# Performance work log

Hardware: AMD Instinct MI355X
Metric: run time of the kernel (lower is better)

## Reference

```python
import jax, jax.numpy as jnp
import numpy as np

HIDDEN = 1024
D_INNER = 2048      # expand * hidden
STATE = 16          # state_dim n
DT_RANK = 64        # ceil(hidden/16)
D_CONV = 4
B, S = 2, 2048
EPS = 1e-5


def setup_inputs() -> dict:
    key = jax.random.key(0)
    ks = jax.random.split(key, 10)
    sc = lambda fan_in: 1.0 / np.sqrt(fan_in)
    x = jax.random.normal(ks[0], (B, S, HIDDEN), dtype=jnp.float32)
    norm_w = jnp.ones((HIDDEN,), dtype=jnp.float32)
    in_proj_w = jax.random.uniform(ks[1], (2 * D_INNER, HIDDEN), minval=-sc(HIDDEN), maxval=sc(HIDDEN), dtype=jnp.float32)
    conv_w = jax.random.uniform(ks[2], (D_INNER, 1, D_CONV), minval=-sc(D_CONV), maxval=sc(D_CONV), dtype=jnp.float32)
    conv_b = jax.random.uniform(ks[3], (D_INNER,), minval=-sc(D_CONV), maxval=sc(D_CONV), dtype=jnp.float32)
    x_proj_w = jax.random.uniform(ks[4], (DT_RANK + 2 * STATE, D_INNER), minval=-sc(D_INNER), maxval=sc(D_INNER), dtype=jnp.float32)
    dt_proj_w = jax.random.uniform(ks[5], (D_INNER, DT_RANK), minval=-sc(DT_RANK), maxval=sc(DT_RANK), dtype=jnp.float32)
    dt_proj_b = jax.random.uniform(ks[6], (D_INNER,), minval=-sc(DT_RANK), maxval=sc(DT_RANK), dtype=jnp.float32)
    A_log = jnp.log(jnp.broadcast_to(jnp.arange(1, STATE + 1, dtype=jnp.float32), (D_INNER, STATE)))
    D = jnp.ones((D_INNER,), dtype=jnp.float32)
    out_proj_w = jax.random.uniform(ks[7], (HIDDEN, D_INNER), minval=-sc(D_INNER), maxval=sc(D_INNER), dtype=jnp.float32)
    return {"x": x, "norm_w": norm_w, "in_proj_w": in_proj_w, "conv_w": conv_w,
            "conv_b": conv_b, "x_proj_w": x_proj_w, "dt_proj_w": dt_proj_w,
            "dt_proj_b": dt_proj_b, "A_log": A_log, "D": D, "out_proj_w": out_proj_w}


def _selective_scan(u, delta, A, Bm, Cm, D):
    # u, delta: [b,s,d]; A: [d,n]; Bm, Cm: [b,s,n]; D: [d]
    deltaA = jnp.exp(jnp.einsum('bsd,dn->bsdn', delta, A))          # [b,s,d,n]
    deltaB_u = jnp.einsum('bsd,bsn,bsd->bsdn', delta, Bm, u)        # [b,s,d,n]

    def step(h, inp):
        dA_t, dBu_t, C_t = inp                                       # [b,d,n],[b,d,n],[b,n]
        h = dA_t * h + dBu_t
        y = jnp.einsum('bdn,bn->bd', h, C_t)
        return h, y

    h0 = jnp.zeros((u.shape[0], u.shape[2], A.shape[1]), dtype=u.dtype)
    _, ys = jax.lax.scan(step, h0,
                         (deltaA.transpose(1, 0, 2, 3),
                          deltaB_u.transpose(1, 0, 2, 3),
                          Cm.transpose(1, 0, 2)))
    y = ys.transpose(1, 0, 2)                                        # [b,s,d]
    return y + u * D


def reference(x, norm_w, in_proj_w, conv_w, conv_b, x_proj_w, dt_proj_w,
              dt_proj_b, A_log, D, out_proj_w):
    # RMSNorm
    xn = x * jax.lax.rsqrt(jnp.mean(x * x, axis=-1, keepdims=True) + EPS) * norm_w

    # in_proj -> split
    x_and_res = xn @ in_proj_w.T                                     # [b,s,2*d_inner]
    xi, res = jnp.split(x_and_res, 2, axis=-1)

    # causal depthwise conv1d (left-pad d_conv-1, truncate to s)
    xc = jax.lax.conv_general_dilated(
        xi.transpose(0, 2, 1), conv_w,
        window_strides=(1,), padding=[(D_CONV - 1, 0)],
        dimension_numbers=('NCH', 'OIH', 'NCH'),
        feature_group_count=D_INNER) + conv_b[None, :, None]
    xc = jax.nn.silu(xc.transpose(0, 2, 1))                          # [b,s,d_inner]

    # ssm
    A = -jnp.exp(A_log)
    x_dbl = xc @ x_proj_w.T                                          # [b,s,dt_rank+2n]
    dt, Bm, Cm = jnp.split(x_dbl, [DT_RANK, DT_RANK + STATE], axis=-1)
    delta = jax.nn.softplus(dt @ dt_proj_w.T + dt_proj_b)            # [b,s,d_inner]
    y = _selective_scan(xc, delta, A, Bm, Cm, D)

    y = y * jax.nn.silu(res)
    out = y @ out_proj_w.T
    return out + x
```

## Files before the change

kernel.cpp:

```cpp
#include <hip/hip_runtime.h>
#include <math.h>

#define HIDDEN   1024
#define D_INNER  2048
#define NSTATE   16
#define DT_RANK  64
#define BATCH    2
#define SEQ      2048
#define T_TOK    (BATCH * SEQ)
#define XDBL     (DT_RANK + 2 * NSTATE)
#define NCH      64
#define CHL      (SEQ / NCH)
#define BDN      (BATCH * D_INNER * NSTATE)

typedef float f32x4   __attribute__((ext_vector_type(4)));
typedef short bf16x8  __attribute__((ext_vector_type(8)));
typedef short short4v __attribute__((ext_vector_type(4)));

#define AS1 __attribute__((address_space(1)))
#define AS3 __attribute__((address_space(3)))
#define GLOAD(src, dst) __builtin_amdgcn_global_load_lds( \
    (const AS1 unsigned int*)(src), (AS3 unsigned int*)(dst), 16, 0, 0)

__device__ __forceinline__ float silu_f(float x) { return x / (1.0f + __expf(-x)); }
__device__ __forceinline__ float softplus_f(float x) {
    return fmaxf(x, 0.0f) + log1pf(__expf(-fabsf(x)));
}
__device__ __forceinline__ unsigned short f2bf(float x) {
    unsigned int u = __float_as_uint(x);
    u += 0x7fffu + ((u >> 16) & 1u);
    return (unsigned short)(u >> 16);
}
__device__ __forceinline__ float bf2f(unsigned short h) {
    return __uint_as_float(((unsigned int)h) << 16);
}

template<int SEGS>
__global__ __launch_bounds__(256) void wpack_kernel(
        const float* __restrict__ w, unsigned short* __restrict__ wp, int K) {
    int i = blockIdx.x * 256 + threadIdx.x;
    int kq = K >> 2;
    int row = i / kq;
    int c = (i - row * kq) << 2;
    float4 v = *(const float4*)(w + (size_t)row * K + c);
    short4v hi, lo;
    hi.x = f2bf(v.x); hi.y = f2bf(v.y); hi.z = f2bf(v.z); hi.w = f2bf(v.w);
    lo.x = f2bf(v.x - bf2f(hi.x)); lo.y = f2bf(v.y - bf2f(hi.y));
    lo.z = f2bf(v.z - bf2f(hi.z)); lo.w = f2bf(v.w - bf2f(hi.w));
    size_t b0 = (size_t)row * (SEGS * K) + c;
    *(short4v*)(wp + b0) = hi;
    if (SEGS == 2) *(short4v*)(wp + b0 + K) = lo;
}

__global__ __launch_bounds__(256) void rmsnorm_pack_kernel(
        const float* __restrict__ x, const float* __restrict__ w,
        unsigned short* __restrict__ xn_p) {
    int row = blockIdx.x;
    float4 v = ((const float4*)(x + (size_t)row * HIDDEN))[threadIdx.x];
    float ss = v.x*v.x + v.y*v.y + v.z*v.z + v.w*v.w;
    #pragma unroll
    for (int off = 32; off; off >>= 1) ss += __shfl_down(ss, off);
    __shared__ float wsum[4];
    if ((threadIdx.x & 63) == 0) wsum[threadIdx.x >> 6] = ss;
    __syncthreads();
    float scale = rsqrtf((wsum[0] + wsum[1] + wsum[2] + wsum[3]) / (float)HIDDEN + 1e-5f);
    float4 wv = ((const float4*)w)[threadIdx.x];
    float o0 = v.x * scale * wv.x, o1 = v.y * scale * wv.y;
    float o2 = v.z * scale * wv.z, o3 = v.w * scale * wv.w;
    short4v hi, lo;
    hi.x = f2bf(o0); hi.y = f2bf(o1); hi.z = f2bf(o2); hi.w = f2bf(o3);
    lo.x = f2bf(o0 - bf2f(hi.x)); lo.y = f2bf(o1 - bf2f(hi.y));
    lo.z = f2bf(o2 - bf2f(hi.z)); lo.w = f2bf(o3 - bf2f(hi.w));
    size_t b0 = (size_t)row * (2 * HIDDEN) + threadIdx.x * 4;
    *(short4v*)&xn_p[b0]          = hi;
    *(short4v*)&xn_p[b0 + HIDDEN] = lo;
}

__global__ __launch_bounds__(256, 2) void mgemm_in_kernel(
        const unsigned short* __restrict__ Ap,
        const unsigned short* __restrict__ Wp,
        float* __restrict__ C0, float* __restrict__ C1) {
    __shared__ short Ah[128 * 64];
    __shared__ short Al[128 * 64];
    __shared__ short Bh[256 * 64];
    const int t = threadIdx.x;
    const int w = t >> 6, l = t & 63;
    const int m0 = blockIdx.y * 128, n0 = blockIdx.x * 256;
    const int lrow = l & 15;
    f32x4 acc[8][4];
    #pragma unroll
    for (int m = 0; m < 8; ++m)
        #pragma unroll
        for (int n = 0; n < 4; ++n) {
            acc[m][n].x = 0.f; acc[m][n].y = 0.f; acc[m][n].z = 0.f; acc[m][n].w = 0.f;
        }
    const int srow8 = l >> 3;
    const int sc8   = (l & 7) ^ srow8;
    const unsigned short* ga = Ap + (size_t)(m0 + w * 32 + srow8) * 2048 + sc8 * 8;
    const unsigned short* gb = Wp + (size_t)(n0 + w * 64 + srow8) * 1024 + sc8 * 8;
    for (int k0 = 0; k0 < 1024; k0 += 64) {
        __syncthreads();
        #pragma unroll
        for (int q = 0; q < 4; ++q) {
            const int ar = (w * 32 + q * 8) * 128;
            GLOAD(ga + k0 + (size_t)q * 8 * 2048,        (char*)Ah + ar);
            GLOAD(ga + 1024 + k0 + (size_t)q * 8 * 2048, (char*)Al + ar);
        }
        #pragma unroll
        for (int q = 0; q < 8; ++q)
            GLOAD(gb + k0 + (size_t)q * 8 * 1024, (char*)Bh + (w * 64 + q * 8) * 128);
        __syncthreads();
        #pragma unroll
        for (int kk = 0; kk < 2; ++kk) {
            const int slot = ((kk * 4 + (l >> 4)) ^ (l & 7)) * 8;
            bf16x8 bh[4];
            #pragma unroll
            for (int n = 0; n < 4; ++n)
                bh[n] = *(const bf16x8*)&Bh[(w * 64 + n * 16 + lrow) * 64 + slot];
            #pragma unroll
            for (int m = 0; m < 8; ++m) {
                bf16x8 ah = *(const bf16x8*)&Ah[(m * 16 + lrow) * 64 + slot];
                bf16x8 al = *(const bf16x8*)&Al[(m * 16 + lrow) * 64 + slot];
                #pragma unroll
                for (int n = 0; n < 4; ++n) {
                    acc[m][n] = __builtin_amdgcn_mfma_f32_16x16x32_bf16(
                        ah, bh[n], acc[m][n], 0, 0, 0);
                    acc[m][n] = __builtin_amdgcn_mfma_f32_16x16x32_bf16(
                        al, bh[n], acc[m][n], 0, 0, 0);
                }
            }
        }
    }
    float* dst = (n0 < D_INNER) ? C0 : C1;
    const int cbase = (n0 < D_INNER) ? n0 : n0 - D_INNER;
    #pragma unroll
    for (int m = 0; m < 8; ++m) {
        #pragma unroll
        for (int n = 0; n < 4; ++n) {
            #pragma unroll
            for (int j = 0; j < 4; ++j) {
                int row = m0 + m * 16 + (l >> 4) * 4 + j;
                int col = cbase + w * 64 + n * 16 + (l & 15);
                dst[(size_t)row * D_INNER + col] = acc[m][n][j];
            }
        }
    }
}

template<int TERMS, int EPI>
__global__ __launch_bounds__(256) void mgemm_kernel(
        const unsigned short* __restrict__ Ap, const unsigned short* __restrict__ Wp,
        int Klog, int klen, int brows, float* __restrict__ C0, float* __restrict__ C1,
        int splitN, int ldout, size_t partStride, const float* __restrict__ bias) {
    constexpr int NT = (TERMS == 3) ? 4 : 3;
    __shared__ short lds[NT * 128 * 64];
    short* Ah = lds;
    short* Al = lds + 128 * 64;
    short* Bh = lds + 2 * 128 * 64;
    short* Bl = lds + 3 * 128 * 64;
    const int t = threadIdx.x;
    const int w = t >> 6, l = t & 63;
    const int m0 = blockIdx.y * 128, n0 = blockIdx.x * 128;
    const int kbeg = blockIdx.z * klen;
    const int wr = (w >> 1) * 64, wc = (w & 1) * 64;
    const int lrow = l & 15;
    f32x4 acc[4][4];
    #pragma unroll
    for (int m = 0; m < 4; ++m)
        #pragma unroll
        for (int n = 0; n < 4; ++n) {
            acc[m][n].x = 0.f; acc[m][n].y = 0.f; acc[m][n].z = 0.f; acc[m][n].w = 0.f;
        }
    const int Asr = 2 * Klog;
    const int Wsr = (TERMS == 3) ? 2 * Klog : Klog;
    const int srow = w * 32 + (l >> 3);
    const int sc8  = (l & 7) ^ ((l >> 3) & 7);
    const int brow = min(n0 + srow, brows - 1);
    const unsigned short* ga = Ap + (size_t)(m0 + srow) * Asr + sc8 * 8;
    const unsigned short* gb = Wp + (size_t)brow * Wsr + sc8 * 8;
    for (int k0 = kbeg; k0 < kbeg + klen; k0 += 64) {
        __syncthreads();
        #pragma unroll
        for (int q = 0; q < 4; ++q) {
            const int doff = (w * 32 + q * 8) * 128;
            GLOAD(ga + k0 + (size_t)q * 8 * Asr,        (char*)Ah + doff);
            GLOAD(ga + Klog + k0 + (size_t)q * 8 * Asr, (char*)Al + doff);
            GLOAD(gb + k0 + (size_t)q * 8 * Wsr,        (char*)Bh + doff);
            if (TERMS == 3)
                GLOAD(gb + Klog + k0 + (size_t)q * 8 * Wsr, (char*)Bl + doff);
        }
        __syncthreads();
        #pragma unroll
        for (int kk = 0; kk < 2; ++kk) {
            const int slot = ((kk * 4 + (l >> 4)) ^ (l & 7)) * 8;
            bf16x8 ah[4], al[4], bh[4], bl[4];
            #pragma unroll
            for (int m = 0; m < 4; ++m) {
                ah[m] = *(const bf16x8*)&Ah[(wr + m * 16 + lrow) * 64 + slot];
                al[m] = *(const bf16x8*)&Al[(wr + m * 16 + lrow) * 64 + slot];
            }
            #pragma unroll
            for (int n = 0; n < 4; ++n) {
                bh[n] = *(const bf16x8*)&Bh[(wc + n * 16 + lrow) * 64 + slot];
                if (TERMS == 3)
                    bl[n] = *(const bf16x8*)&Bl[(wc + n * 16 + lrow) * 64 + slot];
            }
            #pragma unroll
            for (int m = 0; m < 4; ++m)
                #pragma unroll
                for (int n = 0; n < 4; ++n) {
                    acc[m][n] = __builtin_amdgcn_mfma_f32_16x16x32_bf16(
                        ah[m], bh[n], acc[m][n], 0, 0, 0);
                    acc[m][n] = __builtin_amdgcn_mfma_f32_16x16x32_bf16(
                        al[m], bh[n], acc[m][n], 0, 0, 0);
                    if (TERMS == 3)
                        acc[m][n] = __builtin_amdgcn_mfma_f32_16x16x32_bf16(
                            ah[m], bl[n], acc[m][n], 0, 0, 0);
                }
        }
    }
    float* dst = (EPI == 2) ? (C0 + blockIdx.z * partStride) : C0;
    #pragma unroll
    for (int m = 0; m < 4; ++m) {
        #pragma unroll
        for (int n = 0; n < 4; ++n) {
            #pragma unroll
            for (int j = 0; j < 4; ++j) {
                int row = m0 + wr + m * 16 + (l >> 4) * 4 + j;
                int col = n0 + wc + n * 16 + (l & 15);
                float v = acc[m][n][j];
                if (EPI == 2) {
                    dst[(size_t)row * ldout + col] = v;
                } else {
                    C0[(size_t)row * ldout + col] = softplus_f(v + bias[col]);
                }
            }
        }
    }
}

__global__ __launch_bounds__(256) void reduce2_kernel(
        const float* __restrict__ parts, size_t partStride,
        const float* __restrict__ x, float* __restrict__ out) {
    size_t i = (size_t)blockIdx.x * 256 + threadIdx.x;
    float4 a = ((const float4*)(parts))[i];
    float4 b = ((const float4*)(parts + partStride))[i];
    float4 xv = ((const float4*)x)[i];
    float4 o;
    o.x = a.x + b.x + xv.x;
    o.y = a.y + b.y + xv.y;
    o.z = a.z + b.z + xv.z;
    o.w = a.w + b.w + xv.w;
    ((float4*)out)[i] = o;
}

__global__ __launch_bounds__(256) void reduceX_kernel(
        const float* __restrict__ parts, float* __restrict__ xdbl,
        unsigned short* __restrict__ dtp) {
    int i = blockIdx.x * 256 + threadIdx.x;
    int row = i / 24;
    int c = (i - row * 24) * 4;
    float4 s = make_float4(0.f, 0.f, 0.f, 0.f);
    #pragma unroll
    for (int z = 0; z < 8; ++z) {
        float4 a = *(const float4*)(parts + (size_t)z * 524288 + (size_t)row * 128 + c);
        s.x += a.x; s.y += a.y; s.z += a.z; s.w += a.w;
    }
    *(float4*)(xdbl + (size_t)row * XDBL + c) = s;
    if (c < DT_RANK) {
        short4v hi, lo;
        hi.x = f2bf(s.x); hi.y = f2bf(s.y); hi.z = f2bf(s.z); hi.w = f2bf(s.w);
        lo.x = f2bf(s.x - bf2f(hi.x)); lo.y = f2bf(s.y - bf2f(hi.y));
        lo.z = f2bf(s.z - bf2f(hi.z)); lo.w = f2bf(s.w - bf2f(hi.w));
        size_t b0 = (size_t)row * 128 + c;
        *(short4v*)(dtp + b0)      = hi;
        *(short4v*)(dtp + b0 + 64) = lo;
    }
}

__global__ __launch_bounds__(256) void conv_silu_kernel(
        const float* __restrict__ xi, const float* __restrict__ w,
        const float* __restrict__ b, unsigned short* __restrict__ xc_p) {
    size_t i = (size_t)blockIdx.x * 256 + threadIdx.x;
    int d = (int)(i & (D_INNER - 1));
    int tt = (int)(i >> 11);
    int s = tt & (SEQ - 1);
    float4 wv = ((const float4*)w)[d];
    float acc = b[d];
    if (s >= 3) acc += wv.x * xi[i - 3 * D_INNER];
    if (s >= 2) acc += wv.y * xi[i - 2 * D_INNER];
    if (s >= 1) acc += wv.z * xi[i - 1 * D_INNER];
    acc += wv.w * xi[i];
    float o = silu_f(acc);
    unsigned short hi = f2bf(o);
    unsigned short lo = f2bf(o - bf2f(hi));
    size_t o2 = (size_t)tt * (2 * D_INNER) + d;
    xc_p[o2]           = hi;
    xc_p[o2 + D_INNER] = lo;
}


__global__ __launch_bounds__(256) void scanA_kernel(
        const unsigned short* __restrict__ xcp, const float* __restrict__ delta,
        const float* __restrict__ xdbl, const float* __restrict__ A_log,
        float* __restrict__ hpart, float* __restrict__ Pp) {
    const int bid = blockIdx.x;
    const int b    = bid >> 9;
    const int c    = (bid >> 3) & 63;
    const int dblk = bid & 7;
    const int d    = (dblk << 8) + threadIdx.x;
    float adn[NSTATE];
    #pragma unroll
    for (int k = 0; k < 4; ++k) {
        float4 a = *(const float4*)(A_log + d * NSTATE + k * 4);
        adn[k*4+0] = -__expf(a.x); adn[k*4+1] = -__expf(a.y);
        adn[k*4+2] = -__expf(a.z); adn[k*4+3] = -__expf(a.w);
    }
    float h[NSTATE], P[NSTATE];
    #pragma unroll
    for (int n = 0; n < NSTATE; ++n) { h[n] = 0.f; P[n] = 1.f; }
    const int rowbase = b * SEQ + c * CHL;
    #pragma unroll 4
    for (int r = 0; r < CHL; ++r) {
        const int row = rowbase + r;
        const float* brow = xdbl + (size_t)row * XDBL + DT_RANK;
        size_t o2 = (size_t)row * (2 * D_INNER) + d;
        float dl = delta[(size_t)row * D_INNER + d];
        float u  = bf2f(xcp[o2]) + bf2f(xcp[o2 + D_INNER]);
        float du = dl * u;
        #pragma unroll
        for (int n = 0; n < NSTATE; ++n) {
            float dA = __expf(dl * adn[n]);
            h[n] = fmaf(dA, h[n], du * brow[n]);
            P[n] *= dA;
        }
    }
    size_t base = (size_t)c * BDN + (size_t)(b * D_INNER + d) * NSTATE;
    #pragma unroll
    for (int k = 0; k < 4; ++k) {
        *(float4*)(hpart + base + k * 4) = make_float4(h[k*4], h[k*4+1], h[k*4+2], h[k*4+3]);
        *(float4*)(Pp    + base + k * 4) = make_float4(P[k*4], P[k*4+1], P[k*4+2], P[k*4+3]);
    }
}

__global__ __launch_bounds__(256) void scanB_kernel(
        const float* __restrict__ hpart, const float* __restrict__ Pp,
        float* __restrict__ hstart) {
    int idx = blockIdx.x * 256 + threadIdx.x;
    float h = 0.f;
    for (int c = 0; c < NCH; ++c) {
        hstart[(size_t)c * BDN + idx] = h;
        h = fmaf(Pp[(size_t)c * BDN + idx], h, hpart[(size_t)c * BDN + idx]);
    }
}

__global__ __launch_bounds__(256) void scanC_kernel(
        const unsigned short* xcp, const float* __restrict__ delta,
        const float* __restrict__ xdbl, const float* __restrict__ A_log,
        const float* __restrict__ Dp, const float* __restrict__ hstart,
        const float* __restrict__ res, unsigned short* y_p) {
    const int bid = blockIdx.x;
    const int b    = bid >> 9;
    const int c    = (bid >> 3) & 63;
    const int dblk = bid & 7;
    const int d    = (dblk << 8) + threadIdx.x;
    float adn[NSTATE];
    #pragma unroll
    for (int k = 0; k < 4; ++k) {
        float4 a = *(const float4*)(A_log + d * NSTATE + k * 4);
        adn[k*4+0] = -__expf(a.x); adn[k*4+1] = -__expf(a.y);
        adn[k*4+2] = -__expf(a.z); adn[k*4+3] = -__expf(a.w);
    }
    const float Dd = Dp[d];
    float h[NSTATE];
    size_t base = (size_t)c * BDN + (size_t)(b * D_INNER + d) * NSTATE;
    #pragma unroll
    for (int k = 0; k < 4; ++k) {
        float4 hv = *(const float4*)(hstart + base + k * 4);
        h[k*4] = hv.x; h[k*4+1] = hv.y; h[k*4+2] = hv.z; h[k*4+3] = hv.w;
    }
    const int rowbase = b * SEQ + c * CHL;
    #pragma unroll 4
    for (int r = 0; r < CHL; ++r) {
        const int row = rowbase + r;
        const float* brow = xdbl + (size_t)row * XDBL + DT_RANK;
        const float* crow = brow + NSTATE;
        size_t o2 = (size_t)row * (2 * D_INNER) + d;
        float dl = delta[(size_t)row * D_INNER + d];
        float u  = bf2f(xcp[o2]) + bf2f(xcp[o2 + D_INNER]);
        float du = dl * u;
        float ys[4];
        ys[0] = u * Dd; ys[1] = 0.f; ys[2] = 0.f; ys[3] = 0.f;
        #pragma unroll
        for (int n = 0; n < NSTATE; ++n) {
            float dA = __expf(dl * adn[n]);
            h[n] = fmaf(dA, h[n], du * brow[n]);
            ys[n & 3] = fmaf(h[n], crow[n], ys[n & 3]);
        }
        float ysum = (ys[0] + ys[1]) + (ys[2] + ys[3]);
        float rv = res[(size_t)row * D_INNER + d];
        float gv = ysum * silu_f(rv);
        unsigned short hi = f2bf(gv);
        unsigned short lo = f2bf(gv - bf2f(hi));
        y_p[o2]           = hi;
        y_p[o2 + D_INNER] = lo;
    }
}

extern "C" void kernel_launch(void* const* d_in, const int* in_sizes, int n_in,
                              void* d_out, int out_size, void* d_ws, size_t ws_size,
                              hipStream_t stream) {
    const float* x         = (const float*)d_in[0];
    const float* norm_w    = (const float*)d_in[1];
    const float* in_proj_w = (const float*)d_in[2];
    const float* conv_w    = (const float*)d_in[3];
    const float* conv_b    = (const float*)d_in[4];
    const float* x_proj_w  = (const float*)d_in[5];
    const float* dt_proj_w = (const float*)d_in[6];
    const float* dt_proj_b = (const float*)d_in[7];
    const float* A_log     = (const float*)d_in[8];
    const float* Dp        = (const float*)d_in[9];
    const float* out_proj_w= (const float*)d_in[10];
    float* out = (float*)d_out;
    float* ws  = (float*)d_ws;

    const size_t M8 = (size_t)T_TOK * D_INNER;
    float* res   = ws;
    float* delta = res + M8;
    float* xdbl  = delta + M8;
    unsigned short* xn_p   = (unsigned short*)(xdbl + (size_t)T_TOK * XDBL);
    unsigned short* w_in_p = xn_p   + (size_t)4096 * 2048;
    unsigned short* w_out_p= w_in_p + (size_t)4096 * 1024;
    unsigned short* w_xp_p = w_out_p+ (size_t)1024 * 4096;
    unsigned short* w_dt_p = w_xp_p + (size_t)96 * 4096;
    unsigned short* xc_p   = w_dt_p + (size_t)2048 * 128;
    unsigned short* dtp_p  = xc_p   + (size_t)4096 * 4096;
    float* xi    = (float*)(dtp_p + (size_t)4096 * 128);
    float* hpart = xi;
    float* Pp    = xi + (size_t)BDN * NCH;
    float* hstart= (float*)xn_p;
    float* parts_x = delta;
    unsigned short* y_p = xc_p;
    float* parts = ws;
    const size_t partStride = (size_t)T_TOK * HIDDEN;

    wpack_kernel<1><<<4096, 256, 0, stream>>>(in_proj_w,  w_in_p,  HIDDEN);
    wpack_kernel<2><<<2048, 256, 0, stream>>>(out_proj_w, w_out_p, D_INNER);
    wpack_kernel<2><<<192,  256, 0, stream>>>(x_proj_w,   w_xp_p,  D_INNER);
    wpack_kernel<2><<<128,  256, 0, stream>>>(dt_proj_w,  w_dt_p,  DT_RANK);

    rmsnorm_pack_kernel<<<T_TOK, 256, 0, stream>>>(x, norm_w, xn_p);

    {
        dim3 g(4096 / 256, T_TOK / 128, 1);
        mgemm_in_kernel<<<g, 256, 0, stream>>>(xn_p, w_in_p, xi, res);
    }

    conv_silu_kernel<<<(int)(M8 / 256), 256, 0, stream>>>(xi, conv_w, conv_b, xc_p);

    {
        dim3 g(1, T_TOK / 128, 8);
        mgemm_kernel<3, 2><<<g, 256, 0, stream>>>(xc_p, w_xp_p, D_INNER, D_INNER / 8,
                                                  96, parts_x, nullptr, 0, 128, 524288, nullptr);
    }
    reduceX_kernel<<<T_TOK * 24 / 256, 256, 0, stream>>>(parts_x, xdbl, dtp_p);

    {
        dim3 g(D_INNER / 128, T_TOK / 128, 1);
        mgemm_kernel<3, 3><<<g, 256, 0, stream>>>(dtp_p, w_dt_p, DT_RANK, DT_RANK,
                                                  D_INNER, delta, nullptr, 0, D_INNER, 0, dt_proj_b);
    }

    scanA_kernel<<<BATCH * NCH * 8, 256, 0, stream>>>(xc_p, delta, xdbl, A_log, hpart, Pp);
    scanB_kernel<<<BDN / 256, 256, 0, stream>>>(hpart, Pp, hstart);
    scanC_kernel<<<BATCH * NCH * 8, 256, 0, stream>>>(xc_p, delta, xdbl, A_log, Dp, hstart, res, y_p);

    {
        dim3 g(HIDDEN / 128, T_TOK / 128, 2);
        mgemm_kernel<3, 2><<<g, 256, 0, stream>>>(y_p, w_out_p, D_INNER, D_INNER / 2,
                                                  HIDDEN, parts, nullptr, 0, HIDDEN, partStride, nullptr);
    }
    reduce2_kernel<<<(int)(partStride / 4 / 256), 256, 0, stream>>>(parts, partStride, x, out);
}
```

Before: 312.7 us.

## Fuse weight packing, stage scan B/C in LDS, write scan prefix in place

Merges the four weight-pack launches into one kernel that branches on block index. The scan kernels now stage each chunk's B and C vectors in shared memory instead of reading them from global memory every step. scanB writes its prefix states back into hpart in place, which removes the separate hstart buffer. The GEMM template is also changed to always load and multiply the low-bf16 weight term, so TERMS no longer controls it; this adds work to any instantiation that used TERMS==2, though every current call site already uses 3.

```diff
diff --git a/kernel.cpp b/kernel.cpp
--- a/kernel.cpp
+++ b/kernel.cpp
@@ -35,10 +35,9 @@
     return __uint_as_float(((unsigned int)h) << 16);
 }
 
-template<int SEGS>
-__global__ __launch_bounds__(256) void wpack_kernel(
-        const float* __restrict__ w, unsigned short* __restrict__ wp, int K) {
-    int i = blockIdx.x * 256 + threadIdx.x;
+__device__ __forceinline__ void pack_seg(
+        const float* __restrict__ w, unsigned short* __restrict__ wp,
+        int K, int segs, int i) {
     int kq = K >> 2;
     int row = i / kq;
     int c = (i - row * kq) << 2;
@@ -47,9 +46,27 @@
     hi.x = f2bf(v.x); hi.y = f2bf(v.y); hi.z = f2bf(v.z); hi.w = f2bf(v.w);
     lo.x = f2bf(v.x - bf2f(hi.x)); lo.y = f2bf(v.y - bf2f(hi.y));
     lo.z = f2bf(v.z - bf2f(hi.z)); lo.w = f2bf(v.w - bf2f(hi.w));
-    size_t b0 = (size_t)row * (SEGS * K) + c;
+    size_t b0 = (size_t)row * (segs * K) + c;
     *(short4v*)(wp + b0) = hi;
-    if (SEGS == 2) *(short4v*)(wp + b0 + K) = lo;
+    if (segs == 2) *(short4v*)(wp + b0 + K) = lo;
+}
+
+__global__ __launch_bounds__(256) void wpack_all_kernel(
+        const float* __restrict__ win,  unsigned short* __restrict__ pin,
+        const float* __restrict__ wout, unsigned short* __restrict__ pout,
+        const float* __restrict__ wx,   unsigned short* __restrict__ px,
+        const float* __restrict__ wdt,  unsigned short* __restrict__ pdt) {
+    int bid = blockIdx.x;
+    int t = threadIdx.x;
+    if (bid < 4096) {
+        pack_seg(win, pin, HIDDEN, 1, bid * 256 + t);
+    } else if (bid < 6144) {
+        pack_seg(wout, pout, D_INNER, 2, (bid - 4096) * 256 + t);
+    } else if (bid < 6336) {
+        pack_seg(wx, px, D_INNER, 2, (bid - 6144) * 256 + t);
+    } else {
+        pack_seg(wdt, pdt, DT_RANK, 2, (bid - 6336) * 256 + t);
+    }
 }
 
 __global__ __launch_bounds__(256) void rmsnorm_pack_kernel(
@@ -172,7 +189,7 @@
             acc[m][n].x = 0.f; acc[m][n].y = 0.f; acc[m][n].z = 0.f; acc[m][n].w = 0.f;
         }
     const int Asr = 2 * Klog;
-    const int Wsr = (TERMS == 3) ? 2 * Klog : Klog;
+    const int Wsr = 2 * Klog;
     const int srow = w * 32 + (l >> 3);
     const int sc8  = (l & 7) ^ ((l >> 3) & 7);
     const int brow = min(n0 + srow, brows - 1);
@@ -186,8 +203,7 @@
             GLOAD(ga + k0 + (size_t)q * 8 * Asr,        (char*)Ah + doff);
             GLOAD(ga + Klog + k0 + (size_t)q * 8 * Asr, (char*)Al + doff);
             GLOAD(gb + k0 + (size_t)q * 8 * Wsr,        (char*)Bh + doff);
-            if (TERMS == 3)
-                GLOAD(gb + Klog + k0 + (size_t)q * 8 * Wsr, (char*)Bl + doff);
+            GLOAD(gb + Klog + k0 + (size_t)q * 8 * Wsr, (char*)Bl + doff);
         }
         __syncthreads();
         #pragma unroll
@@ -202,8 +218,7 @@
             #pragma unroll
             for (int n = 0; n < 4; ++n) {
                 bh[n] = *(const bf16x8*)&Bh[(wc + n * 16 + lrow) * 64 + slot];
-                if (TERMS == 3)
-                    bl[n] = *(const bf16x8*)&Bl[(wc + n * 16 + lrow) * 64 + slot];
+                bl[n] = *(const bf16x8*)&Bl[(wc + n * 16 + lrow) * 64 + slot];
             }
             #pragma unroll
             for (int m = 0; m < 4; ++m)
@@ -213,9 +228,8 @@
                         ah[m], bh[n], acc[m][n], 0, 0, 0);
                     acc[m][n] = __builtin_amdgcn_mfma_f32_16x16x32_bf16(
                         al[m], bh[n], acc[m][n], 0, 0, 0);
-                    if (TERMS == 3)
-                        acc[m][n] = __builtin_amdgcn_mfma_f32_16x16x32_bf16(
-                            ah[m], bl[n], acc[m][n], 0, 0, 0);
+                    acc[m][n] = __builtin_amdgcn_mfma_f32_16x16x32_bf16(
+                        ah[m], bl[n], acc[m][n], 0, 0, 0);
                 }
         }
     }
@@ -304,11 +318,19 @@
         const unsigned short* __restrict__ xcp, const float* __restrict__ delta,
         const float* __restrict__ xdbl, const float* __restrict__ A_log,
         float* __restrict__ hpart, float* __restrict__ Pp) {
+    __shared__ float sB[CHL * NSTATE];
     const int bid = blockIdx.x;
     const int b    = bid >> 9;
     const int c    = (bid >> 3) & 63;
     const int dblk = bid & 7;
     const int d    = (dblk << 8) + threadIdx.x;
+    const int rowbase = b * SEQ + c * CHL;
+    #pragma unroll
+    for (int q = 0; q < 2; ++q) {
+        int e = threadIdx.x + q * 256;
+        int r = e >> 4, n = e & 15;
+        sB[e] = xdbl[(size_t)(rowbase + r) * XDBL + DT_RANK + n];
+    }
     float adn[NSTATE];
     #pragma unroll
     for (int k = 0; k < 4; ++k) {
@@ -319,11 +341,11 @@
     float h[NSTATE], P[NSTATE];
     #pragma unroll
     for (int n = 0; n < NSTATE; ++n) { h[n] = 0.f; P[n] = 1.f; }
-    const int rowbase = b * SEQ + c * CHL;
+    __syncthreads();
     #pragma unroll 4
     for (int r = 0; r < CHL; ++r) {
         const int row = rowbase + r;
-        const float* brow = xdbl + (size_t)row * XDBL + DT_RANK;
+        const float* brow = &sB[r * NSTATE];
         size_t o2 = (size_t)row * (2 * D_INNER) + d;
         float dl = delta[(size_t)row * D_INNER + d];
         float u  = bf2f(xcp[o2]) + bf2f(xcp[o2 + D_INNER]);
@@ -344,13 +366,15 @@
 }
 
 __global__ __launch_bounds__(256) void scanB_kernel(
-        const float* __restrict__ hpart, const float* __restrict__ Pp,
-        float* __restrict__ hstart) {
+        float* __restrict__ hpart, const float* __restrict__ Pp) {
     int idx = blockIdx.x * 256 + threadIdx.x;
     float h = 0.f;
     for (int c = 0; c < NCH; ++c) {
-        hstart[(size_t)c * BDN + idx] = h;
-        h = fmaf(Pp[(size_t)c * BDN + idx], h, hpart[(size_t)c * BDN + idx]);
+        size_t o = (size_t)c * BDN + idx;
+        float hp = hpart[o];
+        float p  = Pp[o];
+        hpart[o] = h;
+        h = fmaf(p, h, hp);
     }
 }
 
@@ -359,11 +383,21 @@
         const float* __restrict__ xdbl, const float* __restrict__ A_log,
         const float* __restrict__ Dp, const float* __restrict__ hstart,
         const float* __restrict__ res, unsigned short* y_p) {
+    __shared__ float sB[CHL * NSTATE];
+    __shared__ float sC[CHL * NSTATE];
     const int bid = blockIdx.x;
     const int b    = bid >> 9;
     const int c    = (bid >> 3) & 63;
     const int dblk = bid & 7;
     const int d    = (dblk << 8) + threadIdx.x;
+    const int rowbase = b * SEQ + c * CHL;
+    #pragma unroll
+    for (int q = 0; q < 2; ++q) {
+        int e = threadIdx.x + q * 256;
+        int r = e >> 4, n = e & 15;
+        sB[e] = xdbl[(size_t)(rowbase + r) * XDBL + DT_RANK + n];
+        sC[e] = xdbl[(size_t)(rowbase + r) * XDBL + DT_RANK + NSTATE + n];
+    }
     float adn[NSTATE];
     #pragma unroll
     for (int k = 0; k < 4; ++k) {
@@ -379,12 +413,12 @@
         float4 hv = *(const float4*)(hstart + base + k * 4);
         h[k*4] = hv.x; h[k*4+1] = hv.y; h[k*4+2] = hv.z; h[k*4+3] = hv.w;
     }
-    const int rowbase = b * SEQ + c * CHL;
+    __syncthreads();
     #pragma unroll 4
     for (int r = 0; r < CHL; ++r) {
         const int row = rowbase + r;
-        const float* brow = xdbl + (size_t)row * XDBL + DT_RANK;
-        const float* crow = brow + NSTATE;
+        const float* brow = &sB[r * NSTATE];
+        const float* crow = &sC[r * NSTATE];
         size_t o2 = (size_t)row * (2 * D_INNER) + d;
         float dl = delta[(size_t)row * D_INNER + d];
         float u  = bf2f(xcp[o2]) + bf2f(xcp[o2 + D_INNER]);
@@ -438,16 +472,13 @@
     float* xi    = (float*)(dtp_p + (size_t)4096 * 128);
     float* hpart = xi;
     float* Pp    = xi + (size_t)BDN * NCH;
-    float* hstart= (float*)xn_p;
     float* parts_x = delta;
     unsigned short* y_p = xc_p;
     float* parts = ws;
     const size_t partStride = (size_t)T_TOK * HIDDEN;
 
-    wpack_kernel<1><<<4096, 256, 0, stream>>>(in_proj_w,  w_in_p,  HIDDEN);
-    wpack_kernel<2><<<2048, 256, 0, stream>>>(out_proj_w, w_out_p, D_INNER);
-    wpack_kernel<2><<<192,  256, 0, stream>>>(x_proj_w,   w_xp_p,  D_INNER);
-    wpack_kernel<2><<<128,  256, 0, stream>>>(dt_proj_w,  w_dt_p,  DT_RANK);
+    wpack_all_kernel<<<6464, 256, 0, stream>>>(in_proj_w, w_in_p, out_proj_w, w_out_p,
+                                               x_proj_w, w_xp_p, dt_proj_w, w_dt_p);
 
     rmsnorm_pack_kernel<<<T_TOK, 256, 0, stream>>>(x, norm_w, xn_p);
 
@@ -472,8 +503,9 @@
     }
 
     scanA_kernel<<<BATCH * NCH * 8, 256, 0, stream>>>(xc_p, delta, xdbl, A_log, hpart, Pp);
-    scanB_kernel<<<BDN / 256, 256, 0, stream>>>(hpart, Pp, hstart);
-    scanC_kernel<<<BATCH * NCH * 8, 256, 0, stream>>>(xc_p, delta, xdbl, A_log, Dp, hstart, res, y_p);
+    scanB_kernel<<<BDN / 256, 256, 0, stream>>>(hpart, Pp);
+    scanC_kernel<<<BATCH * NCH * 8, 256, 0, stream>>>(xc_p, delta, xdbl, A_log, Dp,
+                                                      hpart, res, y_p);
 
     {
         dim3 g(HIDDEN / 128, T_TOK / 128, 2);
```

Measured after the change: 303.8 us. 1.03x faster.
